# Kernel tuning notes

Hardware: AMD Instinct MI355X
Metric: run time of the kernel (lower is better)

The kernel has to match this reference:

```python
import jax, jax.numpy as jnp
import numpy as np

RANK, A1, A2, B1, B2 = 64, 64, 64, 64, 64
N_TOKENS = 8192


def _xavier_uniform(key, shape, fan_in, fan_out, dtype=jnp.float32):
    bound = float(np.sqrt(6.0 / (fan_in + fan_out)))
    return jax.random.uniform(key, shape, dtype, -bound, bound)


def setup_inputs() -> dict:
    key = jax.random.key(0)
    kx, ka, kb, kbias = jax.random.split(key, 4)
    x = jax.random.normal(kx, (N_TOKENS, A1 * B1), dtype=jnp.float32)
    # torch xavier on a 3D tensor (rank, d1, d2): fan_in = d1*d2, fan_out = rank*d2
    a = _xavier_uniform(ka, (RANK, A1, A2), A1 * A2, RANK * A2)
    b = _xavier_uniform(kb, (RANK, B1, B2), B1 * B2, RANK * B2)
    bias = jax.random.normal(kbias, (A2 * B2,), dtype=jnp.float32)
    return {"x": x, "a": a, "b": b, "bias": bias}


def reference(x, a, b, bias):
    r, a1, a2 = a.shape
    _, b1, b2 = b.shape
    # w = sum_r kron(a_r, b_r):  w[i*b1+k, j*b2+l] = sum_r a[r,i,j] * b[r,k,l]
    w = jnp.einsum('rij,rkl->ikjl', a, b).reshape(a1 * b1, a2 * b2)
    out = x @ w  # (N, a2*b2)
    return out + bias[None, :]
```

## Files before the change

### kernel.cpp

```cpp
#include <hip/hip_runtime.h>
#include <hip/hip_bf16.h>


#define M_DIM 8192
#define N_DIM 4096
#define K_DIM 4096
#define KT_COUNT 128

typedef __attribute__((ext_vector_type(8))) short short8;
typedef __attribute__((ext_vector_type(4))) short short4v;
typedef __attribute__((ext_vector_type(4))) float floatx4;
typedef __attribute__((ext_vector_type(16))) float floatx16;

typedef __attribute__((address_space(1))) void gvoid_t;
typedef __attribute__((address_space(3))) void lvoid_t;

static __device__ __forceinline__ void gl_lds16(const void* g, const void* l) {
  __builtin_amdgcn_global_load_lds((gvoid_t*)(unsigned long long)g,
                                   (lvoid_t*)(unsigned int)(unsigned long long)l,
                                   16, 0, 0);
}

static __device__ __forceinline__ unsigned short f2bf(float f) {
  unsigned int u = __builtin_bit_cast(unsigned int, f);
  u = (u + 0x7fffu + ((u >> 16) & 1u)) >> 16;
  return (unsigned short)u;
}

__global__ __launch_bounds__(256) void prep_kernel(
    const float* __restrict__ x, const float* __restrict__ a,
    const float* __restrict__ b, unsigned short* __restrict__ Xp,
    unsigned short* __restrict__ Wp) {
  __shared__ float lds[128 * 33];
  const int bid = blockIdx.x;
  const int t = threadIdx.x;

  if (bid < 1024) {
    const int i = bid >> 4;
    const int k0 = (bid & 15) * 4;

    {
#pragma unroll
      for (int q = 0; q < 4; ++q) {
        const int idx = q * 256 + t;
        const int r = idx >> 4, jq = idx & 15;
        float4 v = ((const float4*)(a + (size_t)r * 4096 + i * 64))[jq];
        ((float4*)lds)[r * 16 + jq] = v;
      }
    }
    __syncthreads();

    const int l = t & 63;
    const int jset = t >> 6;
    float acc[16][4];
#pragma unroll
    for (int jj = 0; jj < 16; ++jj)
#pragma unroll
      for (int kb = 0; kb < 4; ++kb) acc[jj][kb] = 0.f;

    const float* bb = b + k0 * 64 + l;
#pragma unroll 2
    for (int r = 0; r < 64; ++r) {
      float bv[4];
#pragma unroll
      for (int kb = 0; kb < 4; ++kb) bv[kb] = bb[(size_t)r * 4096 + kb * 64];
      float av[16];
#pragma unroll
      for (int jq = 0; jq < 4; ++jq) {
        float4 aj = ((const float4*)lds)[r * 16 + jset * 4 + jq];
        av[jq * 4 + 0] = aj.x; av[jq * 4 + 1] = aj.y;
        av[jq * 4 + 2] = aj.z; av[jq * 4 + 3] = aj.w;
      }
#pragma unroll
      for (int jj = 0; jj < 16; ++jj)
#pragma unroll
        for (int kb = 0; kb < 4; ++kb)
          acc[jj][kb] = fmaf(av[jj], bv[kb], acc[jj][kb]);
    }

    const int kt = (i * 64 + k0) >> 5;
    const int c = (k0 & 31) >> 3;
    const int half = (k0 >> 2) & 1;
#pragma unroll
    for (int jj = 0; jj < 16; ++jj) {
      const int j = jset * 16 + jj;
      const int n = j * 64 + l;
      const int blob = (n >> 7) * KT_COUNT + kt;
      const int pos = c * 128 + (n & 127);
      short4v o;
#pragma unroll
      for (int kb = 0; kb < 4; ++kb) o[kb] = (short)f2bf(acc[jj][kb]);
      *(short4v*)(Wp + (size_t)blob * 4096 + pos * 8 + half * 4) = o;
    }
  } else {
    const int pid = bid - 1024;
    const int kt = pid & 127;
    const int M0 = pid >> 7;

    {
      const int row = t >> 1;
      const int half = t & 1;
      const float* src = x + (size_t)(M0 * 128 + row) * K_DIM + kt * 32 + half * 16;
      float v[16];
#pragma unroll
      for (int w = 0; w < 4; ++w) {
        float4 vv = ((const float4*)src)[w];
        v[w * 4 + 0] = vv.x; v[w * 4 + 1] = vv.y;
        v[w * 4 + 2] = vv.z; v[w * 4 + 3] = vv.w;
      }
#pragma unroll
      for (int e = 0; e < 16; ++e) lds[row * 33 + half * 16 + e] = v[e];
    }
    __syncthreads();

    unsigned short* dst = Xp + (size_t)(M0 * KT_COUNT + kt) * 4096;
#pragma unroll
    for (int q = 0; q < 2; ++q) {
      const int p = q * 256 + t;
      const int c = p >> 7, mm = p & 127;
      short8 o;
#pragma unroll
      for (int j = 0; j < 8; ++j) o[j] = (short)f2bf(lds[mm * 33 + c * 8 + j]);
      *(short8*)(dst + p * 8) = o;
    }
  }
}

__global__ __launch_bounds__(256) void gemm_kernel(
    const unsigned short* __restrict__ Xp, const unsigned short* __restrict__ Wp,
    const float* __restrict__ bias, float* __restrict__ out) {
  __shared__ short8 As[512];
  __shared__ short8 Bs[512];

  const int bid = blockIdx.x;
  const int xcd = bid & 7;
  const int pos = bid >> 3;
  const int N0 = xcd * 4 + (pos & 3);
  const int M0 = pos >> 2;

  const int t = threadIdx.x;
  const int wave = t >> 6, lane = t & 63;
  const int l32 = lane & 31, hl = lane >> 5;
  const int wm = wave & 1, wn = wave >> 1;

  floatx16 acc[2][2];
#pragma unroll
  for (int mt = 0; mt < 2; ++mt)
#pragma unroll
    for (int nt = 0; nt < 2; ++nt)
#pragma unroll
      for (int r = 0; r < 16; ++r) acc[mt][nt][r] = 0.f;

  const unsigned short* pa = Xp + (size_t)M0 * KT_COUNT * 4096 + (size_t)t * 8;
  const unsigned short* pb = Wp + (size_t)N0 * KT_COUNT * 4096 + (size_t)t * 8;
  const short8* lA0 = As + wave * 64;
  const short8* lA1 = As + 256 + wave * 64;
  const short8* lB0 = Bs + wave * 64;
  const short8* lB1 = Bs + 256 + wave * 64;

  for (int kt = 0; kt < KT_COUNT; ++kt) {
    __syncthreads();
    gl_lds16(pa, lA0);
    gl_lds16(pa + 2048, lA1);
    gl_lds16(pb, lB0);
    gl_lds16(pb + 2048, lB1);
    pa += 4096;
    pb += 4096;
    __syncthreads();

#pragma unroll
    for (int ks = 0; ks < 2; ++ks) {
      const int c = ks * 2 + hl;
      short8 af[2], bf[2];
#pragma unroll
      for (int mt = 0; mt < 2; ++mt)
        af[mt] = As[c * 128 + wm * 64 + mt * 32 + l32];
#pragma unroll
      for (int nt = 0; nt < 2; ++nt)
        bf[nt] = Bs[c * 128 + wn * 64 + nt * 32 + l32];
#pragma unroll
      for (int mt = 0; mt < 2; ++mt)
#pragma unroll
        for (int nt = 0; nt < 2; ++nt)
          acc[mt][nt] = __builtin_amdgcn_mfma_f32_32x32x16_bf16(
              af[mt], bf[nt], acc[mt][nt], 0, 0, 0);
    }
  }

  const int col_base = N0 * 128 + wn * 64;
  const int row_base = M0 * 128 + wm * 64 + 4 * hl;
#pragma unroll
  for (int nt = 0; nt < 2; ++nt) {
    const int col = col_base + nt * 32 + l32;
    const float bv = bias[col];
#pragma unroll
    for (int mt = 0; mt < 2; ++mt) {
      floatx16 v = acc[mt][nt];
#pragma unroll
      for (int r = 0; r < 16; ++r) {
        const int row = row_base + mt * 32 + (r & 3) + 8 * (r >> 2);
        out[(size_t)row * N_DIM + col] = v[r] + bv;
      }
    }
  }
}

extern "C" void kernel_launch(void* const* d_in, const int* in_sizes, int n_in,
                              void* d_out, int out_size, void* d_ws, size_t ws_size,
                              hipStream_t stream) {
  const float* x = (const float*)d_in[0];
  const float* a = (const float*)d_in[1];
  const float* b = (const float*)d_in[2];
  const float* bias = (const float*)d_in[3];
  float* out = (float*)d_out;

  unsigned short* Xp = (unsigned short*)d_ws;
  unsigned short* Wp = Xp + (size_t)M_DIM * K_DIM;

  prep_kernel<<<1024 + 8192, 256, 0, stream>>>(x, a, b, Xp, Wp);
  gemm_kernel<<<2048, 256, 0, stream>>>(Xp, Wp, bias, out);
}
```

Before: 576.5 us.

## Switch GEMM to 16x16x32 MFMA with 64-deep K tiles per barrier

```diff
diff --git a/kernel.cpp b/kernel.cpp
--- a/kernel.cpp
+++ b/kernel.cpp
@@ -10,7 +10,6 @@
 typedef __attribute__((ext_vector_type(8))) short short8;
 typedef __attribute__((ext_vector_type(4))) short short4v;
 typedef __attribute__((ext_vector_type(4))) float floatx4;
-typedef __attribute__((ext_vector_type(16))) float floatx16;
 
 typedef __attribute__((address_space(1))) void gvoid_t;
 typedef __attribute__((address_space(3))) void lvoid_t;
@@ -129,8 +128,8 @@
 __global__ __launch_bounds__(256) void gemm_kernel(
     const unsigned short* __restrict__ Xp, const unsigned short* __restrict__ Wp,
     const float* __restrict__ bias, float* __restrict__ out) {
-  __shared__ short8 As[512];
-  __shared__ short8 Bs[512];
+  __shared__ short8 As[1024];
+  __shared__ short8 Bs[1024];
 
   const int bid = blockIdx.x;
   const int xcd = bid & 7;
@@ -140,66 +139,60 @@
 
   const int t = threadIdx.x;
   const int wave = t >> 6, lane = t & 63;
-  const int l32 = lane & 31, hl = lane >> 5;
+  const int l16 = lane & 15, quad = lane >> 4;
   const int wm = wave & 1, wn = wave >> 1;
 
-  floatx16 acc[2][2];
-#pragma unroll
-  for (int mt = 0; mt < 2; ++mt)
-#pragma unroll
-    for (int nt = 0; nt < 2; ++nt)
-#pragma unroll
-      for (int r = 0; r < 16; ++r) acc[mt][nt][r] = 0.f;
+  floatx4 acc[4][4];
+#pragma unroll
+  for (int mt = 0; mt < 4; ++mt)
+#pragma unroll
+    for (int nt = 0; nt < 4; ++nt) acc[mt][nt] = (floatx4){0.f, 0.f, 0.f, 0.f};
 
   const unsigned short* pa = Xp + (size_t)M0 * KT_COUNT * 4096 + (size_t)t * 8;
   const unsigned short* pb = Wp + (size_t)N0 * KT_COUNT * 4096 + (size_t)t * 8;
-  const short8* lA0 = As + wave * 64;
-  const short8* lA1 = As + 256 + wave * 64;
-  const short8* lB0 = Bs + wave * 64;
-  const short8* lB1 = Bs + 256 + wave * 64;
-
-  for (int kt = 0; kt < KT_COUNT; ++kt) {
-    __syncthreads();
-    gl_lds16(pa, lA0);
-    gl_lds16(pa + 2048, lA1);
-    gl_lds16(pb, lB0);
-    gl_lds16(pb + 2048, lB1);
-    pa += 4096;
-    pb += 4096;
+
+  for (int kt = 0; kt < KT_COUNT / 2; ++kt) {
+    __syncthreads();
+#pragma unroll
+    for (int q = 0; q < 4; ++q) {
+      gl_lds16(pa + q * 2048, As + wave * 64 + q * 256);
+      gl_lds16(pb + q * 2048, Bs + wave * 64 + q * 256);
+    }
+    pa += 8192;
+    pb += 8192;
     __syncthreads();
 
 #pragma unroll
     for (int ks = 0; ks < 2; ++ks) {
-      const int c = ks * 2 + hl;
-      short8 af[2], bf[2];
-#pragma unroll
-      for (int mt = 0; mt < 2; ++mt)
-        af[mt] = As[c * 128 + wm * 64 + mt * 32 + l32];
-#pragma unroll
-      for (int nt = 0; nt < 2; ++nt)
-        bf[nt] = Bs[c * 128 + wn * 64 + nt * 32 + l32];
-#pragma unroll
-      for (int mt = 0; mt < 2; ++mt)
-#pragma unroll
-        for (int nt = 0; nt < 2; ++nt)
-          acc[mt][nt] = __builtin_amdgcn_mfma_f32_32x32x16_bf16(
+      short8 af[4], bf[4];
+#pragma unroll
+      for (int mt = 0; mt < 4; ++mt)
+        af[mt] = As[ks * 512 + quad * 128 + wm * 64 + mt * 16 + l16];
+#pragma unroll
+      for (int nt = 0; nt < 4; ++nt)
+        bf[nt] = Bs[ks * 512 + quad * 128 + wn * 64 + nt * 16 + l16];
+#pragma unroll
+      for (int mt = 0; mt < 4; ++mt)
+#pragma unroll
+        for (int nt = 0; nt < 4; ++nt)
+          acc[mt][nt] = __builtin_amdgcn_mfma_f32_16x16x32_bf16(
               af[mt], bf[nt], acc[mt][nt], 0, 0, 0);
     }
   }
 
   const int col_base = N0 * 128 + wn * 64;
-  const int row_base = M0 * 128 + wm * 64 + 4 * hl;
-#pragma unroll
-  for (int nt = 0; nt < 2; ++nt) {
-    const int col = col_base + nt * 32 + l32;
+  const int row_base = M0 * 128 + wm * 64;
+#pragma unroll
+  for (int nt = 0; nt < 4; ++nt) {
+    const int col = col_base + nt * 16 + l16;
     const float bv = bias[col];
 #pragma unroll
-    for (int mt = 0; mt < 2; ++mt) {
-      floatx16 v = acc[mt][nt];
-#pragma unroll
-      for (int r = 0; r < 16; ++r) {
-        const int row = row_base + mt * 32 + (r & 3) + 8 * (r >> 2);
-        out[(size_t)row * N_DIM + col] = v[r] + bv;
+    for (int mt = 0; mt < 4; ++mt) {
+      floatx4 v = acc[mt][nt];
+#pragma unroll
+      for (int r4 = 0; r4 < 4; ++r4) {
+        const int row = row_base + mt * 16 + quad * 4 + r4;
+        out[(size_t)row * N_DIM + col] = v[r4] + bv;
       }
     }
   }
```

Measured after the change: 531.7 us. 1.08x faster.
